# Kernel optimization log

Hardware: AMD Instinct MI355X
Metric: run time of the kernel (lower is better)

The kernel has to match this reference:

```python
import jax, jax.numpy as jnp
import numpy as np

N_NODES = 100000
IN_DIM = 256
OUT_DIM = 128
N_EDGES = 3200000


def setup_inputs() -> dict:
    key = jax.random.key(0)
    k1, k2, k3, k4, k5, k6 = jax.random.split(key, 6)
    stdv = 1.0 / np.sqrt(OUT_DIM)
    return {
        "feature_map": jax.random.normal(k1, (N_NODES, IN_DIM), dtype=jnp.float32),
        "edge_src": jax.random.randint(k2, (N_EDGES,), 0, N_NODES, dtype=jnp.int32),
        "edge_dst": jax.random.randint(k3, (N_EDGES,), 0, N_NODES, dtype=jnp.int32),
        "edge_vals": jax.random.uniform(k4, (N_EDGES,), dtype=jnp.float32),
        "weights": jax.random.uniform(k5, (IN_DIM, OUT_DIM), dtype=jnp.float32, minval=-stdv, maxval=stdv),
        "b": jax.random.uniform(k6, (OUT_DIM,), dtype=jnp.float32, minval=-stdv, maxval=stdv),
    }


def reference(feature_map, edge_src, edge_dst, edge_vals, weights, b):
    # dense feature transform: [N, in] @ [in, out] -> [N, out]
    h = feature_map @ weights
    # sparse adjacency matmul A @ h via edge list:
    # out[dst] += A[dst, src] * h[src]
    msgs = edge_vals[:, None] * h[edge_src]  # [E, out]
    out = jax.ops.segment_sum(msgs, edge_dst, num_segments=N_NODES)
    # fused bias add epilogue
    return out + b
```

## Files before the change

### kernel.cpp

```cpp
#include <hip/hip_runtime.h>

#define N_NODES 100000
#define IN_DIM 256
#define OUT_DIM 128
#define N_EDGES 3200000

#define NB 1563
#define CAP 2560
#define PTILE 6400
#define PBLK 500
#define GBLK 782

typedef __attribute__((ext_vector_type(8))) short short8;
typedef __attribute__((ext_vector_type(4))) float float4v;

__device__ __forceinline__ unsigned short f2bf(float f) {
    union { float f; unsigned int u; } v; v.f = f;
    unsigned int r = v.u + 0x7FFF + ((v.u >> 16) & 1);
    return (unsigned short)(r >> 16);
}

__global__ __launch_bounds__(256) void setup_kernel(const float* __restrict__ W,
                                                    unsigned short* __restrict__ Wf,
                                                    int* __restrict__ cursor) {
    if (blockIdx.x < 16) {
        const int f = blockIdx.x * 256 + threadIdx.x;
        const int lane = f & 63;
        const int qc = f >> 6;
        const int q = qc >> 3, ct = qc & 7;
        const int n = ct * 16 + (lane & 15);
        const int k0 = q * 32 + (lane >> 4) * 8;
        unsigned int o[4];
#pragma unroll
        for (int jj = 0; jj < 4; ++jj) {
            const unsigned short lo = f2bf(W[(k0 + 2 * jj) * OUT_DIM + n]);
            const unsigned short hi = f2bf(W[(k0 + 2 * jj + 1) * OUT_DIM + n]);
            o[jj] = (unsigned)lo | ((unsigned)hi << 16);
        }
        ((uint4*)Wf)[f] = make_uint4(o[0], o[1], o[2], o[3]);
    } else {
        const int i = (blockIdx.x - 16) * 256 + threadIdx.x;
        if (i < NB) cursor[i] = 0;
    }
}

__global__ __launch_bounds__(512, 4) void fused_kernel(const float* __restrict__ X,
                                                       const unsigned short* __restrict__ Wf,
                                                       unsigned short* __restrict__ hb,
                                                       const int* __restrict__ src,
                                                       const int* __restrict__ dst,
                                                       const float* __restrict__ vals,
                                                       int* __restrict__ cursor,
                                                       int2* __restrict__ pairs) {
    __shared__ int smem[8192];
    const int tid = threadIdx.x;

    if (blockIdx.x < PBLK) {
        int* lhist = smem;
        int* lbase = smem + NB;
        const int base = blockIdx.x * PTILE;
        const int lim = base + PTILE;

        for (int i = tid; i < NB; i += 512) lhist[i] = 0;
        __syncthreads();

#pragma unroll
        for (int k = 0; k < 13; ++k) {
            const int e = base + tid + k * 512;
            if (e < lim) atomicAdd(&lhist[dst[e] >> 6], 1);
        }
        __syncthreads();

        for (int i = tid; i < NB; i += 512) {
            const int c = lhist[i];
            if (c) lbase[i] = atomicAdd(&cursor[i], c);
        }
        __syncthreads();
        for (int i = tid; i < NB; i += 512) lhist[i] = 0;
        __syncthreads();

#pragma unroll
        for (int k = 0; k < 13; ++k) {
            const int e = base + tid + k * 512;
            if (e < lim) {
                const int d = dst[e];
                const int b = d >> 6;
                const int r = atomicAdd(&lhist[b], 1);
                const int pos = lbase[b] + r;
                if (pos < CAP)
                    pairs[(long)b * CAP + pos] =
                        make_int2(src[e] | ((d & 63) << 20), __float_as_int(vals[e]));
            }
        }
    } else {
        const int bid = blockIdx.x - PBLK;
        const int wid = tid >> 6;
        const int lane = tid & 63;
        const int m = lane & 15;
        const int quad = lane >> 4;
        const int row0 = bid * 128 + wid * 16;

        const int rl = min(row0 + m, N_NODES - 1);
        const float* xr = X + (long)rl * IN_DIM + quad * 8;
        short8 afrag[8];
#pragma unroll
        for (int q = 0; q < 8; ++q) {
            const float4 xa = *(const float4*)(xr + q * 32);
            const float4 xb = *(const float4*)(xr + q * 32 + 4);
            short8 f;
            f[0] = (short)f2bf(xa.x); f[1] = (short)f2bf(xa.y);
            f[2] = (short)f2bf(xa.z); f[3] = (short)f2bf(xa.w);
            f[4] = (short)f2bf(xb.x); f[5] = (short)f2bf(xb.y);
            f[6] = (short)f2bf(xb.z); f[7] = (short)f2bf(xb.w);
            afrag[q] = f;
        }

        unsigned short* stage = (unsigned short*)smem + wid * 2048;
        const short8* wfrag = (const short8*)Wf;
#pragma unroll 1
        for (int ct = 0; ct < 8; ++ct) {
            float4v acc = {0.f, 0.f, 0.f, 0.f};
#pragma unroll
            for (int q = 0; q < 8; ++q) {
                const short8 bfr = wfrag[(q * 8 + ct) * 64 + lane];
                acc = __builtin_amdgcn_mfma_f32_16x16x32_bf16(afrag[q], bfr, acc, 0, 0, 0);
            }
#pragma unroll
            for (int r = 0; r < 4; ++r)
                stage[(quad * 4 + r) * 128 + ct * 16 + m] = f2bf(acc[r]);
        }

#pragma unroll
        for (int j = 0; j < 4; ++j) {
            const uint4 vdata = *(const uint4*)(stage + j * 512 + lane * 8);
            const int row_r = row0 + j * 4 + quad;
            if (row_r < N_NODES)
                *(uint4*)(hb + (long)row_r * OUT_DIM + m * 8) = vdata;
        }
    }
}

__global__ __launch_bounds__(256) void gather_kernel(const int* __restrict__ cursor,
                                                     const int2* __restrict__ pairs,
                                                     const unsigned short* __restrict__ hb,
                                                     const float* __restrict__ bias,
                                                     float* __restrict__ out) {
    __shared__ int2 lp[CAP];
    __shared__ int rcnt[64];
    __shared__ int rbase[64];
    const int blk = blockIdx.x;
    const int tid = threadIdx.x;
    const int wid = tid >> 6;
    const int lane = tid & 63;
    const int c = lane * 2;

    const long beg = (long)blk * CAP;
    const int cnt = min(cursor[blk], CAP);

    if (tid < 64) rcnt[tid] = 0;
    __syncthreads();

    int2 sp[10];
    int  sr[10];
#pragma unroll
    for (int k = 0; k < 10; ++k) {
        const int i = tid + k * 256;
        sr[k] = -1;
        if (i < cnt) {
            const int2 p = pairs[beg + i];
            const int r = (p.x >> 20) & 63;
            const int rk = atomicAdd(&rcnt[r], 1);
            sp[k] = p;
            sr[k] = (r << 13) | rk;
        }
    }
    __syncthreads();

    if (wid == 0) {
        const int v = rcnt[lane];
        int incl = v;
#pragma unroll
        for (int off = 1; off < 64; off <<= 1) {
            const int t = __shfl_up(incl, off);
            if (lane >= off) incl += t;
        }
        rbase[lane] = incl - v;
    }
    __syncthreads();

#pragma unroll
    for (int k = 0; k < 10; ++k) {
        if (sr[k] >= 0)
            lp[rbase[sr[k] >> 13] + (sr[k] & 0x1FFF)] = sp[k];
    }
    __syncthreads();

    const float2 bb = *(const float2*)(bias + c);
#pragma unroll 1
    for (int rr = 0; rr < 16; ++rr) {
        const int r = wid * 16 + rr;
        const int node = blk * 64 + r;
        if (node >= N_NODES) break;
        const int rb = rbase[r];
        const int re = rb + rcnt[r];

        float2 acc[8];
#pragma unroll
        for (int t = 0; t < 8; ++t) acc[t] = make_float2(0.f, 0.f);

        int j = rb;
        for (; j + 7 < re; j += 8) {
            int2 p[8];
            unsigned u[8];
#pragma unroll
            for (int t = 0; t < 8; ++t) p[t] = lp[j + t];
#pragma unroll
            for (int t = 0; t < 8; ++t)
                u[t] = *(const unsigned*)(hb + (long)(p[t].x & 0xFFFFF) * OUT_DIM + c);
#pragma unroll
            for (int t = 0; t < 8; ++t) {
                const float v = __int_as_float(p[t].y);
                acc[t].x += v * __uint_as_float(u[t] << 16);
                acc[t].y += v * __uint_as_float(u[t] & 0xFFFF0000u);
            }
        }
        for (; j < re; ++j) {
            const int2 p0 = lp[j];
            const unsigned u0 = *(const unsigned*)(hb + (long)(p0.x & 0xFFFFF) * OUT_DIM + c);
            const float v0 = __int_as_float(p0.y);
            acc[0].x += v0 * __uint_as_float(u0 << 16);
            acc[0].y += v0 * __uint_as_float(u0 & 0xFFFF0000u);
        }
        float2 o;
        o.x = bb.x + ((acc[0].x + acc[1].x) + (acc[2].x + acc[3].x))
                   + ((acc[4].x + acc[5].x) + (acc[6].x + acc[7].x));
        o.y = bb.y + ((acc[0].y + acc[1].y) + (acc[2].y + acc[3].y))
                   + ((acc[4].y + acc[5].y) + (acc[6].y + acc[7].y));
        *(float2*)(out + (long)node * OUT_DIM + c) = o;
    }
}

extern "C" void kernel_launch(void* const* d_in, const int* in_sizes, int n_in,
                              void* d_out, int out_size, void* d_ws, size_t ws_size,
                              hipStream_t stream) {
    const float* X     = (const float*)d_in[0];
    const int*   esrc  = (const int*)d_in[1];
    const int*   edst  = (const int*)d_in[2];
    const float* evals = (const float*)d_in[3];
    const float* W     = (const float*)d_in[4];
    const float* b     = (const float*)d_in[5];
    float* out = (float*)d_out;

    char* ws = (char*)d_ws;
    unsigned short* hb = (unsigned short*)(ws);
    int2* pairs        = (int2*)(ws + 25600000);
    int*  cursor       = (int*) (ws + 25600000 + 32010240);
    unsigned short* Wf = (unsigned short*)(ws + 57616496);

    setup_kernel<<<dim3(23), dim3(256), 0, stream>>>(W, Wf, cursor);
    fused_kernel<<<dim3(PBLK + GBLK), dim3(512), 0, stream>>>(X, Wf, hb,
                                                              esrc, edst, evals,
                                                              cursor, pairs);
    gather_kernel<<<dim3(NB), dim3(256), 0, stream>>>(cursor, pairs, hb, b, out);
}
```

Baseline: 397.9 us.

## Interleave partition and GEMM blocks, cache edges in registers, deepen gather unroll

Partition blocks and GEMM blocks of the fused kernel are now interleaved by block index, so both kinds of work run together on the GPU instead of partition blocks being scheduled first. The partition pass loads dst/src/vals once, keeps them in registers with the local rank from the first atomic, and drops the second histogram pass, its reset and a sync. This halves the global edge reads and the LDS atomics. The aggregation loop adds a 16-wide unrolled gather to keep more loads in flight, at the cost of extra register pressure.

Result: faster. 360.3 us (-9.5%).

```diff
diff --git a/kernel.cpp b/kernel.cpp
--- a/kernel.cpp
+++ b/kernel.cpp
@@ -54,20 +54,33 @@
                                                        int2* __restrict__ pairs) {
     __shared__ int smem[8192];
     const int tid = threadIdx.x;
-
-    if (blockIdx.x < PBLK) {
+    const int bx = blockIdx.x;
+    const bool is_part = (bx < 1000) && ((bx & 1) == 0);
+
+    if (is_part) {
         int* lhist = smem;
         int* lbase = smem + NB;
-        const int base = blockIdx.x * PTILE;
-        const int lim = base + PTILE;
+        const int pid = bx >> 1;
+        const int base = pid * PTILE;
 
         for (int i = tid; i < NB; i += 512) lhist[i] = 0;
         __syncthreads();
 
+        int   pk[13];
+        int   sv[13];
+        float vv[13];
 #pragma unroll
         for (int k = 0; k < 13; ++k) {
             const int e = base + tid + k * 512;
-            if (e < lim) atomicAdd(&lhist[dst[e] >> 6], 1);
+            pk[k] = -1;
+            if (tid + k * 512 < PTILE) {
+                const int d = dst[e];
+                const int b = d >> 6;
+                const int r = atomicAdd(&lhist[b], 1);
+                pk[k] = (b << 19) | (r << 6) | (d & 63);
+                sv[k] = src[e];
+                vv[k] = vals[e];
+            }
         }
         __syncthreads();
 
@@ -76,29 +89,25 @@
             if (c) lbase[i] = atomicAdd(&cursor[i], c);
         }
         __syncthreads();
-        for (int i = tid; i < NB; i += 512) lhist[i] = 0;
-        __syncthreads();
 
 #pragma unroll
         for (int k = 0; k < 13; ++k) {
-            const int e = base + tid + k * 512;
-            if (e < lim) {
-                const int d = dst[e];
-                const int b = d >> 6;
-                const int r = atomicAdd(&lhist[b], 1);
+            if (pk[k] >= 0) {
+                const int b = pk[k] >> 19;
+                const int r = (pk[k] >> 6) & 0x1FFF;
                 const int pos = lbase[b] + r;
                 if (pos < CAP)
                     pairs[(long)b * CAP + pos] =
-                        make_int2(src[e] | ((d & 63) << 20), __float_as_int(vals[e]));
+                        make_int2(sv[k] | ((pk[k] & 63) << 20), __float_as_int(vv[k]));
             }
         }
     } else {
-        const int bid = blockIdx.x - PBLK;
+        const int gid = (bx < 1000) ? (bx >> 1) : (bx - 500);
         const int wid = tid >> 6;
         const int lane = tid & 63;
         const int m = lane & 15;
         const int quad = lane >> 4;
-        const int row0 = bid * 128 + wid * 16;
+        const int row0 = gid * 128 + wid * 16;
 
         const int rl = min(row0 + m, N_NODES - 1);
         const float* xr = X + (long)rl * IN_DIM + quad * 8;
@@ -209,6 +218,21 @@
         for (int t = 0; t < 8; ++t) acc[t] = make_float2(0.f, 0.f);
 
         int j = rb;
+        for (; j + 15 < re; j += 16) {
+            int2 p[16];
+            unsigned u[16];
+#pragma unroll
+            for (int t = 0; t < 16; ++t) p[t] = lp[j + t];
+#pragma unroll
+            for (int t = 0; t < 16; ++t)
+                u[t] = *(const unsigned*)(hb + (long)(p[t].x & 0xFFFFF) * OUT_DIM + c);
+#pragma unroll
+            for (int t = 0; t < 16; ++t) {
+                const float v = __int_as_float(p[t].y);
+                acc[t & 7].x += v * __uint_as_float(u[t] << 16);
+                acc[t & 7].y += v * __uint_as_float(u[t] & 0xFFFF0000u);
+            }
+        }
         for (; j + 7 < re; j += 8) {
             int2 p[8];
             unsigned u[8];
```
